# Kernel tuning notes

Measured on AMD Instinct MI355X. Metric: run time of the kernel, lower is better.

## Reference

```python
import jax, jax.numpy as jnp
import numpy as np
import math

B, S, D, H, FF, NB = 32, 512, 512, 8, 2048, 2
DK = D // H  # 64
NEG = -1e30  # stands in for torch's -1e32 (fp32-safe)


def _make_pe():
    # CosinePositionalEmbedding: deterministic sin/cos part (the 0.1*randn is fully overwritten)
    pos = np.arange(S, dtype=np.float32)[:, None]
    div = np.exp(np.arange(0, D, 2, dtype=np.float32) * -(math.log(10000.0) / D))
    pe = np.zeros((S, D), np.float32)
    pe[:, 0::2] = np.sin(pos * div)
    pe[:, 1::2] = np.cos(pos * div)
    return jnp.asarray(pe)[None]  # [1, S, D]


def setup_inputs() -> dict:
    key = jax.random.key(0)
    ks = jax.random.split(key, 10)
    def w(k, shape):
        return jax.random.normal(k, shape, jnp.float32) * 0.02
    return {
        "q_embed_data": jax.random.normal(ks[0], (B, S, D), jnp.float32),
        "qa_embed_data": jax.random.normal(ks[1], (B, S, D), jnp.float32),
        "forget_rate": jax.random.uniform(ks[2], (B, 1, S, 1), jnp.float32),
        "pe": _make_pe(),
        "Wk": w(ks[3], (NB, D, D)), "bk": jnp.zeros((NB, D), jnp.float32),
        "Wv": w(ks[4], (NB, D, D)), "bv": jnp.zeros((NB, D), jnp.float32),
        "Wo": w(ks[5], (NB, D, D)), "bo": jnp.zeros((NB, D), jnp.float32),
        "g1": jnp.ones((NB, D), jnp.float32), "be1": jnp.zeros((NB, D), jnp.float32),
        "W1": w(ks[6], (NB, D, FF)), "bf1": jnp.zeros((NB, FF), jnp.float32),
        "W2": w(ks[7], (NB, FF, D)), "bf2": jnp.zeros((NB, D), jnp.float32),
        "g2": jnp.ones((NB, D), jnp.float32), "be2": jnp.zeros((NB, D), jnp.float32),
    }


def _ln(x, g, b):
    m = jnp.mean(x, axis=-1, keepdims=True)
    v = jnp.var(x, axis=-1, keepdims=True)
    return (x - m) * jax.lax.rsqrt(v + 1e-5) * g + b


def reference(q_embed_data, qa_embed_data, forget_rate, pe, Wk, bk, Wv, bv, Wo, bo,
              g1, be1, W1, bf1, W2, bf2, g2, be2):
    x = q_embed_data + pe[:, :S]   # query stream
    y = qa_embed_data + pe[:, :S]  # value stream (constant across blocks)
    # mask==0 path: src_mask True where triu(k=0)==0, i.e. strictly-past positions j < i
    allowed = jnp.tril(jnp.ones((S, S), bool), k=-1)
    scale = 1.0 / math.sqrt(DK)
    for i in range(NB):
        # kq_same=True: q and k both use k_linear; query=key=x so q == k
        q = (x @ Wk[i] + bk[i]).reshape(B, S, H, DK).transpose(0, 2, 1, 3)  # [B,H,S,dk]
        k = q
        v = (y @ Wv[i] + bv[i]).reshape(B, S, H, DK).transpose(0, 2, 1, 3)
        scores = jnp.einsum('bhqd,bhkd->bhqk', q, k) * scale      # [B,H,S,S]
        scores = scores * forget_rate                              # broadcast [B,1,S,1]
        scores = jnp.where(allowed, scores, NEG)                   # masked_fill(mask==0, -1e32)
        attn = jax.nn.softmax(scores, axis=-1)
        attn = attn.at[:, :, 0, :].set(0.0)                        # zero_pad first query row
        out = jnp.einsum('bhqk,bhkd->bhqd', attn, v)
        out = out.transpose(0, 2, 1, 3).reshape(B, S, D) @ Wo[i] + bo[i]
        x = _ln(x + out, g1[i], be1[i])
        ffn = jax.nn.relu(x @ W1[i] + bf1[i]) @ W2[i] + bf2[i]
        x = _ln(x + ffn, g2[i], be2[i])
    return x
```

## Files before the change

kernel.cpp:

```cpp
#include <hip/hip_runtime.h>

#define B_ 32
#define S_ 512
#define D_ 512
#define H_ 8
#define DK_ 64
#define FF_ 2048

typedef float f32x4 __attribute__((ext_vector_type(4)));
typedef __bf16 bf16x8 __attribute__((ext_vector_type(8)));
typedef __bf16 bf16x4 __attribute__((ext_vector_type(4)));

__device__ __forceinline__ void gld_lds16(const void* gptr, void* lptr) {
    auto g = (__attribute__((address_space(1))) void*)(unsigned long long)gptr;
    auto l = (__attribute__((address_space(3))) void*)(unsigned)(unsigned long long)lptr;
    __builtin_amdgcn_global_load_lds(g, l, 16, 0, 0);
}

__global__ __launch_bounds__(256) void prep_kernel(
    const float* __restrict__ q, const float* __restrict__ qa,
    const float* __restrict__ pe, __bf16* __restrict__ xbf,
    __bf16* __restrict__ ybf)
{
    const int n4 = B_ * S_ * D_ / 4;
    for (int i = blockIdx.x * blockDim.x + threadIdx.x; i < n4;
         i += gridDim.x * blockDim.x) {
        float4 pv = ((const float4*)pe)[i & (S_ * D_ / 4 - 1)];
        float4 qv = ((const float4*)q)[i];
        float4 av = ((const float4*)qa)[i];
        bf16x4 xb = {(__bf16)(qv.x + pv.x), (__bf16)(qv.y + pv.y),
                     (__bf16)(qv.z + pv.z), (__bf16)(qv.w + pv.w)};
        ((bf16x4*)xbf)[i] = xb;
        bf16x4 yb = {(__bf16)(av.x + pv.x), (__bf16)(av.y + pv.y),
                     (__bf16)(av.z + pv.z), (__bf16)(av.w + pv.w)};
        ((bf16x4*)ybf)[i] = yb;
    }
}

__device__ __forceinline__ void ttile(
    const float* __restrict__ in, __bf16* __restrict__ out,
    int R, int C, int bx, int by, int t)
{
    __shared__ float tile[32][33];
    const int tc = bx * 32, tr = by * 32;
    const int lx = t & 31, ly = t >> 5;
    #pragma unroll
    for (int yy = ly; yy < 32; yy += 8)
        tile[yy][lx] = in[(long)(tr + yy) * C + tc + lx];
    __syncthreads();
    #pragma unroll
    for (int yy = ly; yy < 32; yy += 8)
        out[(long)(tc + yy) * R + tr + lx] = (__bf16)tile[lx][yy];
}

__global__ __launch_bounds__(256) void transpose6(
    const float* __restrict__ Wk, const float* __restrict__ Wv,
    const float* __restrict__ Wo, __bf16* __restrict__ ok,
    __bf16* __restrict__ ov, __bf16* __restrict__ oo)
{
    const int z = blockIdx.z, sel = z >> 1, i = z & 1;
    const float* src = sel == 0 ? Wk : (sel == 1 ? Wv : Wo);
    __bf16* dst = sel == 0 ? ok : (sel == 1 ? ov : oo);
    ttile(src + (long)i * 262144, dst + (long)i * 262144, 512, 512,
          blockIdx.x, blockIdx.y, threadIdx.x);
}

__global__ __launch_bounds__(256) void transposeW1(
    const float* __restrict__ W1, __bf16* __restrict__ o1)
{
    const int i = blockIdx.z;
    ttile(W1 + (long)i * 1048576, o1 + (long)i * 1048576, 512, 2048,
          blockIdx.x, blockIdx.y, threadIdx.x);
}

__global__ __launch_bounds__(256) void transposeW2(
    const float* __restrict__ W2, __bf16* __restrict__ o2)
{
    const int i = blockIdx.z;
    ttile(W2 + (long)i * 1048576, o2 + (long)i * 1048576, 2048, 512,
          blockIdx.x, blockIdx.y, threadIdx.x);
}

__global__ __launch_bounds__(256) void vtrans_kernel(
    const __bf16* __restrict__ V, __bf16* __restrict__ Vt)
{
    __shared__ __bf16 tile[64][72];
    const int sb = blockIdx.x, h = blockIdx.y, b = blockIdx.z;
    const int t = threadIdx.x;
    #pragma unroll
    for (int it = 0; it < 16; ++it) {
        int idx = it * 256 + t;
        int rr = idx >> 6, cc = idx & 63;
        tile[cc][rr] = V[((long)(b * S_ + sb * 64 + rr)) * D_ + h * DK_ + cc];
    }
    __syncthreads();
    #pragma unroll
    for (int it = 0; it < 16; ++it) {
        int idx = it * 256 + t;
        int dd = idx >> 6, so = idx & 63;
        Vt[((long)(b * H_ + h) * DK_ + dd) * S_ + sb * 64 + so] = tile[dd][so];
    }
}

template <int RELU, int MODE>
__global__ __launch_bounds__(256) void gemm_kernel(
    const __bf16* __restrict__ A, const __bf16* __restrict__ Bt,
    const float* __restrict__ bias, const __bf16* __restrict__ res,
    __bf16* __restrict__ out, int M, int N, int K)
{
    __shared__ __bf16 As[2][128 * 64];
    __shared__ __bf16 Bs[2][128 * 64];
    const int t = threadIdx.x;
    const int lane = t & 63;
    const int wv = t >> 6, wr = wv >> 1, wc = wv & 1;
    const int lr = lane & 15, lk = lane >> 4;

    const int nwg = gridDim.x * gridDim.y;
    const int lin = blockIdx.y * gridDim.x + blockIdx.x;
    const int swz = (lin & 7) * (nwg >> 3) + (lin >> 3);
    const int m0 = (swz / gridDim.x) * 128, n0 = (swz % gridDim.x) * 128;

    const int srow = t >> 3;
    const int sslot = (t & 7) ^ (srow & 7);
    const __bf16* gA = A + (long)(m0 + srow) * K + sslot * 8;
    const __bf16* gB = Bt + (long)(n0 + srow) * K + sslot * 8;
    const long rstep = (long)32 * K;

    auto STAGE = [&](int bsel, int k0) {
        char* ldsA = (char*)As[bsel] + t * 16;
        char* ldsB = (char*)Bs[bsel] + t * 16;
        #pragma unroll
        for (int u = 0; u < 4; ++u) {
            gld_lds16(gA + u * rstep + k0, ldsA + u * 4096);
            gld_lds16(gB + u * rstep + k0, ldsB + u * 4096);
        }
    };

    f32x4 acc[4][4] = {};
    auto COMPUTE = [&](int bsel) {
        #pragma unroll
        for (int kk = 0; kk < 2; ++kk) {
            bf16x8 af[4], bfr[4];
            #pragma unroll
            for (int i = 0; i < 4; ++i) {
                const int rr = wr * 64 + i * 16 + lr;
                af[i] = *(const bf16x8*)((const char*)As[bsel] +
                        (rr << 7) + (((kk * 4 + lk) ^ (rr & 7)) << 4));
            }
            #pragma unroll
            for (int j = 0; j < 4; ++j) {
                const int rr = wc * 64 + j * 16 + lr;
                bfr[j] = *(const bf16x8*)((const char*)Bs[bsel] +
                         (rr << 7) + (((kk * 4 + lk) ^ (rr & 7)) << 4));
            }
            #pragma unroll
            for (int i = 0; i < 4; ++i)
                #pragma unroll
                for (int j = 0; j < 4; ++j)
                    acc[i][j] = __builtin_amdgcn_mfma_f32_16x16x32_bf16(
                        bfr[j], af[i], acc[i][j], 0, 0, 0);
        }
    };

    const int NT = K >> 6;
    STAGE(0, 0);
    STAGE(1, 64);
    for (int kt = 0; kt < NT - 1; ++kt) {
        asm volatile("s_waitcnt vmcnt(8)" ::: "memory");
        __builtin_amdgcn_s_barrier();
        COMPUTE(kt & 1);
        __builtin_amdgcn_s_barrier();
        if (kt + 2 < NT) STAGE(kt & 1, (kt + 2) << 6);
    }
    asm volatile("s_waitcnt vmcnt(0)" ::: "memory");
    __builtin_amdgcn_s_barrier();
    COMPUTE((NT - 1) & 1);

    #pragma unroll
    for (int i = 0; i < 4; ++i) {
        const int m = m0 + wr * 64 + i * 16 + lr;
        #pragma unroll
        for (int j = 0; j < 4; ++j) {
            const int nb = n0 + wc * 64 + j * 16 + lk * 4;
            const float4 bv = *(const float4*)(bias + nb);
            float v0 = acc[i][j][0] + bv.x;
            float v1 = acc[i][j][1] + bv.y;
            float v2 = acc[i][j][2] + bv.z;
            float v3 = acc[i][j][3] + bv.w;
            if (MODE == 1) {
                const bf16x4 rv = *(const bf16x4*)(res + (long)m * N + nb);
                v0 += (float)rv[0]; v1 += (float)rv[1];
                v2 += (float)rv[2]; v3 += (float)rv[3];
            }
            if (RELU) {
                v0 = v0 > 0.f ? v0 : 0.f; v1 = v1 > 0.f ? v1 : 0.f;
                v2 = v2 > 0.f ? v2 : 0.f; v3 = v3 > 0.f ? v3 : 0.f;
            }
            bf16x4 ov = {(__bf16)v0, (__bf16)v1, (__bf16)v2, (__bf16)v3};
            *(bf16x4*)(out + (long)m * N + nb) = ov;
        }
    }
}

__global__ __launch_bounds__(256) void attn_kernel(
    const __bf16* __restrict__ Q, const __bf16* __restrict__ Vt,
    const float* __restrict__ fr, __bf16* __restrict__ Out)
{
    __shared__ __bf16 Ks[64 * 64];
    __shared__ __bf16 Vs[64 * 64];
    __shared__ __bf16 Plds[4][16 * 64];
    const int t = threadIdx.x;
    const int lane = t & 63, wv = t >> 6;
    const int lr = lane & 15, lk = lane >> 4;
    const int qb = blockIdx.x, h = blockIdx.y, b = blockIdx.z;
    const int qT = qb * 64 + wv * 16;

    const __bf16* qp = Q + (long)(b * S_ + qT + lr) * D_ + h * DK_ + lk * 8;
    const bf16x8 qf0 = *(const bf16x8*)qp;
    const bf16x8 qf1 = *(const bf16x8*)(qp + 32);

    float frv[4], ls[4];
    #pragma unroll
    for (int r = 0; r < 4; ++r) {
        frv[r] = fr[b * S_ + qT + lk * 4 + r] * 0.125f;
        ls[r] = 0.f;
    }
    f32x4 o[4] = {};

    const int srow = t >> 3;
    const int sslot = (t & 7) ^ (srow & 7);
    const __bf16* kstage = Q + (long)(b * S_ + srow) * D_ + h * DK_ + sslot * 8;
    const __bf16* vstage = Vt + ((long)(b * H_ + h) * DK_ + srow) * S_ + sslot * 8;
    char* kd = (char*)Ks + t * 16;
    char* vd = (char*)Vs + t * 16;
    __bf16* pl = &Plds[wv][0];
    const int sw = (lr & 7);

    for (int ks = 0; ks <= qb * 64; ks += 64) {
        gld_lds16(kstage + (long)ks * D_, kd);
        gld_lds16(kstage + (long)(ks + 32) * D_, kd + 4096);
        gld_lds16(vstage + ks, vd);
        gld_lds16(vstage + ks + 32 * S_, vd + 4096);
        __syncthreads();

        f32x4 s[4] = {};
        #pragma unroll
        for (int j = 0; j < 4; ++j) {
            const char* kb = (const char*)Ks + ((j * 16 + lr) << 7);
            const bf16x8 kf0 = *(const bf16x8*)(kb + ((lk ^ sw) << 4));
            const bf16x8 kf1 = *(const bf16x8*)(kb + (((lk + 4) ^ sw) << 4));
            s[j] = __builtin_amdgcn_mfma_f32_16x16x32_bf16(qf0, kf0, s[j], 0, 0, 0);
            s[j] = __builtin_amdgcn_mfma_f32_16x16x32_bf16(qf1, kf1, s[j], 0, 0, 0);
        }
        #pragma unroll
        for (int j = 0; j < 4; ++j) {
            const int col = ks + j * 16 + lr;
            const int c8 = j * 2 + (lr >> 3), cb = lr & 7;
            #pragma unroll
            for (int r = 0; r < 4; ++r) {
                const int row = lk * 4 + r;
                const int sidx = row * 64 + ((c8 ^ (row & 7)) << 3) + cb;
                const float e = __expf(s[j][r] * frv[r]);
                const float p = (col < qT + row) ? e : 0.f;
                ls[r] += p;
                pl[sidx] = (__bf16)p;
            }
        }
        bf16x8 pf[2];
        #pragma unroll
        for (int kk = 0; kk < 2; ++kk) {
            const int ridx = lr * 64 + (((kk * 4 + lk) ^ sw) << 3);
            pf[kk] = *(const bf16x8*)&pl[ridx];
        }
        #pragma unroll
        for (int dt = 0; dt < 4; ++dt) {
            const char* vb = (const char*)Vs + ((dt * 16 + lr) << 7);
            #pragma unroll
            for (int kk = 0; kk < 2; ++kk) {
                const bf16x8 vf = *(const bf16x8*)(vb + (((kk * 4 + lk) ^ sw) << 4));
                o[dt] = __builtin_amdgcn_mfma_f32_16x16x32_bf16(pf[kk], vf, o[dt], 0, 0, 0);
            }
        }
        __syncthreads();
    }

    #pragma unroll
    for (int r = 0; r < 4; ++r) {
        #pragma unroll
        for (int d = 1; d < 16; d <<= 1)
            ls[r] += __shfl_xor(ls[r], d);
        const float inv = ls[r] > 0.f ? 1.f / ls[r] : 0.f;
        #pragma unroll
        for (int dt = 0; dt < 4; ++dt)
            Out[(long)(b * S_ + qT + lk * 4 + r) * D_ + h * DK_ + dt * 16 + lr] =
                (__bf16)(o[dt][r] * inv);
    }
}

__global__ __launch_bounds__(256) void ln_kernel(
    const __bf16* __restrict__ pre, const float* __restrict__ g,
    const float* __restrict__ be, float* __restrict__ xout,
    __bf16* __restrict__ xbf, int wf32)
{
    const int lane = threadIdx.x & 63, wv = threadIdx.x >> 6;
    const long row = (long)blockIdx.x * 4 + wv;
    const bf16x8 v = *(const bf16x8*)(pre + row * D_ + lane * 8);
    float f[8];
    #pragma unroll
    for (int k = 0; k < 8; ++k) f[k] = (float)v[k];
    float s = 0.f, ss = 0.f;
    #pragma unroll
    for (int k = 0; k < 8; ++k) { s += f[k]; ss += f[k] * f[k]; }
    #pragma unroll
    for (int d = 1; d < 64; d <<= 1) {
        s  += __shfl_xor(s, d);
        ss += __shfl_xor(ss, d);
    }
    const float mean = s * (1.f / 512.f);
    const float rstd = rsqrtf(ss * (1.f / 512.f) - mean * mean + 1e-5f);
    const float4 ga = ((const float4*)(g + lane * 8))[0];
    const float4 gc = ((const float4*)(g + lane * 8))[1];
    const float4 ba = ((const float4*)(be + lane * 8))[0];
    const float4 bc = ((const float4*)(be + lane * 8))[1];
    float o[8];
    o[0] = (f[0] - mean) * rstd * ga.x + ba.x;
    o[1] = (f[1] - mean) * rstd * ga.y + ba.y;
    o[2] = (f[2] - mean) * rstd * ga.z + ba.z;
    o[3] = (f[3] - mean) * rstd * ga.w + ba.w;
    o[4] = (f[4] - mean) * rstd * gc.x + bc.x;
    o[5] = (f[5] - mean) * rstd * gc.y + bc.y;
    o[6] = (f[6] - mean) * rstd * gc.z + bc.z;
    o[7] = (f[7] - mean) * rstd * gc.w + bc.w;
    bf16x8 xb = {(__bf16)o[0], (__bf16)o[1], (__bf16)o[2], (__bf16)o[3],
                 (__bf16)o[4], (__bf16)o[5], (__bf16)o[6], (__bf16)o[7]};
    *(bf16x8*)(xbf + row * D_ + lane * 8) = xb;
    if (wf32) {
        float* xo = xout + row * D_ + lane * 8;
        ((float4*)xo)[0] = make_float4(o[0], o[1], o[2], o[3]);
        ((float4*)xo)[1] = make_float4(o[4], o[5], o[6], o[7]);
    }
}

extern "C" void kernel_launch(void* const* d_in, const int* in_sizes, int n_in,
                              void* d_out, int out_size, void* d_ws, size_t ws_size,
                              hipStream_t stream) {
    const float* q_embed = (const float*)d_in[0];
    const float* qa_embed = (const float*)d_in[1];
    const float* fr  = (const float*)d_in[2];
    const float* pe  = (const float*)d_in[3];
    const float* Wk  = (const float*)d_in[4];
    const float* bk  = (const float*)d_in[5];
    const float* Wv  = (const float*)d_in[6];
    const float* bv  = (const float*)d_in[7];
    const float* Wo  = (const float*)d_in[8];
    const float* bo  = (const float*)d_in[9];
    const float* g1  = (const float*)d_in[10];
    const float* be1 = (const float*)d_in[11];
    const float* W1  = (const float*)d_in[12];
    const float* bf1 = (const float*)d_in[13];
    const float* W2  = (const float*)d_in[14];
    const float* bf2 = (const float*)d_in[15];
    const float* g2  = (const float*)d_in[16];
    const float* be2 = (const float*)d_in[17];

    char* ws = (char*)d_ws;
    __bf16* xbf   = (__bf16*)(ws + 0);
    __bf16* ybf   = (__bf16*)(ws + 16777216);
    __bf16* pool  = (__bf16*)(ws + 33554432);
    __bf16* preln = (__bf16*)(ws + 100663296);
    __bf16* wts   = (__bf16*)(ws + 117440512);

    __bf16* kbuf  = pool;
    __bf16* vbuf  = pool + 8388608;
    __bf16* vtbuf = pool + 2 * 8388608;
    __bf16* abuf  = pool + 3 * 8388608;
    __bf16* f1buf = pool;

    __bf16* wkt = wts;
    __bf16* wvt = wts + 524288;
    __bf16* wot = wts + 1048576;
    __bf16* w1t = wts + 1572864;
    __bf16* w2t = wts + 3670016;

    transpose6 <<<dim3(16, 16, 6), 256, 0, stream>>>(Wk, Wv, Wo, wkt, wvt, wot);
    transposeW1<<<dim3(64, 16, 2), 256, 0, stream>>>(W1, w1t);
    transposeW2<<<dim3(16, 64, 2), 256, 0, stream>>>(W2, w2t);
    prep_kernel<<<2048, 256, 0, stream>>>(q_embed, qa_embed, pe, xbf, ybf);

    for (int i = 0; i < 2; ++i) {
        gemm_kernel<0, 0><<<dim3(4, 128), 256, 0, stream>>>(
            xbf, wkt + i * 262144, bk + i * 512, nullptr, kbuf, 16384, 512, 512);
        gemm_kernel<0, 0><<<dim3(4, 128), 256, 0, stream>>>(
            ybf, wvt + i * 262144, bv + i * 512, nullptr, vbuf, 16384, 512, 512);
        vtrans_kernel<<<dim3(8, 8, 32), 256, 0, stream>>>(vbuf, vtbuf);
        attn_kernel<<<dim3(8, 8, 32), 256, 0, stream>>>(kbuf, vtbuf, fr, abuf);
        gemm_kernel<0, 1><<<dim3(4, 128), 256, 0, stream>>>(
            abuf, wot + i * 262144, bo + i * 512, xbf, preln, 16384, 512, 512);
        ln_kernel<<<4096, 256, 0, stream>>>(preln, g1 + i * 512, be1 + i * 512,
                                            (float*)d_out, xbf, 0);
        gemm_kernel<1, 0><<<dim3(16, 128), 256, 0, stream>>>(
            xbf, w1t + i * 1048576, bf1 + i * 2048, nullptr, f1buf, 16384, 2048, 512);
        gemm_kernel<0, 1><<<dim3(4, 128), 256, 0, stream>>>(
            f1buf, w2t + i * 1048576, bf2 + i * 512, xbf, preln, 16384, 512, 2048);
        ln_kernel<<<4096, 256, 0, stream>>>(preln, g2 + i * 512, be2 + i * 512,
                                            (float*)d_out, xbf, i == 1 ? 1 : 0);
    }
}
```

Baseline: 491.2 us.

## Fuse V transpose into V-projection GEMM epilogue via swapped MFMA operands

The V projection GEMM gets a new epilogue mode that writes its output directly in the per-head transposed layout used by attention, removing the separate transpose kernel and its intermediate buffer. To support that, the MFMA operand order is swapped so each lane holds consecutive rows, which changes the epilogue for all GEMMs to scalar bf16 stores and residual loads strided by N. This saves one launch and a full read/write pass of V, but risks less coalesced stores in every other GEMM, including the large FFN ones.

```diff
diff --git a/kernel.cpp b/kernel.cpp
--- a/kernel.cpp
+++ b/kernel.cpp
@@ -81,27 +81,6 @@
           blockIdx.x, blockIdx.y, threadIdx.x);
 }
 
-__global__ __launch_bounds__(256) void vtrans_kernel(
-    const __bf16* __restrict__ V, __bf16* __restrict__ Vt)
-{
-    __shared__ __bf16 tile[64][72];
-    const int sb = blockIdx.x, h = blockIdx.y, b = blockIdx.z;
-    const int t = threadIdx.x;
-    #pragma unroll
-    for (int it = 0; it < 16; ++it) {
-        int idx = it * 256 + t;
-        int rr = idx >> 6, cc = idx & 63;
-        tile[cc][rr] = V[((long)(b * S_ + sb * 64 + rr)) * D_ + h * DK_ + cc];
-    }
-    __syncthreads();
-    #pragma unroll
-    for (int it = 0; it < 16; ++it) {
-        int idx = it * 256 + t;
-        int dd = idx >> 6, so = idx & 63;
-        Vt[((long)(b * H_ + h) * DK_ + dd) * S_ + sb * 64 + so] = tile[dd][so];
-    }
-}
-
 template <int RELU, int MODE>
 __global__ __launch_bounds__(256) void gemm_kernel(
     const __bf16* __restrict__ A, const __bf16* __restrict__ Bt,
@@ -158,7 +137,7 @@
                 #pragma unroll
                 for (int j = 0; j < 4; ++j)
                     acc[i][j] = __builtin_amdgcn_mfma_f32_16x16x32_bf16(
-                        bfr[j], af[i], acc[i][j], 0, 0, 0);
+                        af[i], bfr[j], acc[i][j], 0, 0, 0);
         }
     };
 
@@ -178,26 +157,29 @@
 
     #pragma unroll
     for (int i = 0; i < 4; ++i) {
-        const int m = m0 + wr * 64 + i * 16 + lr;
         #pragma unroll
         for (int j = 0; j < 4; ++j) {
-            const int nb = n0 + wc * 64 + j * 16 + lk * 4;
-            const float4 bv = *(const float4*)(bias + nb);
-            float v0 = acc[i][j][0] + bv.x;
-            float v1 = acc[i][j][1] + bv.y;
-            float v2 = acc[i][j][2] + bv.z;
-            float v3 = acc[i][j][3] + bv.w;
-            if (MODE == 1) {
-                const bf16x4 rv = *(const bf16x4*)(res + (long)m * N + nb);
-                v0 += (float)rv[0]; v1 += (float)rv[1];
-                v2 += (float)rv[2]; v3 += (float)rv[3];
-            }
-            if (RELU) {
-                v0 = v0 > 0.f ? v0 : 0.f; v1 = v1 > 0.f ? v1 : 0.f;
-                v2 = v2 > 0.f ? v2 : 0.f; v3 = v3 > 0.f ? v3 : 0.f;
-            }
-            bf16x4 ov = {(__bf16)v0, (__bf16)v1, (__bf16)v2, (__bf16)v3};
-            *(bf16x4*)(out + (long)m * N + nb) = ov;
+            const int n = n0 + wc * 64 + j * 16 + lr;
+            const float bv = bias[n];
+            if (MODE == 2) {
+                const int mb = m0 + wr * 64 + i * 16 + lk * 4;
+                const int b = mb >> 9, s = mb & 511;
+                bf16x4 ov = {(__bf16)(acc[i][j][0] + bv),
+                             (__bf16)(acc[i][j][1] + bv),
+                             (__bf16)(acc[i][j][2] + bv),
+                             (__bf16)(acc[i][j][3] + bv)};
+                *(bf16x4*)(out + (((long)(b * 8 + (n >> 6)) * 64 + (n & 63)) << 9) + s) = ov;
+            } else {
+                #pragma unroll
+                for (int r = 0; r < 4; ++r) {
+                    const int m = m0 + wr * 64 + i * 16 + lk * 4 + r;
+                    const long off = (long)m * N + n;
+                    float v = acc[i][j][r] + bv;
+                    if (MODE == 1) v += (float)res[off];
+                    if (RELU) v = v > 0.f ? v : 0.f;
+                    out[off] = (__bf16)v;
+                }
+            }
         }
     }
 }
@@ -371,9 +353,8 @@
     __bf16* wts   = (__bf16*)(ws + 117440512);
 
     __bf16* kbuf  = pool;
-    __bf16* vbuf  = pool + 8388608;
-    __bf16* vtbuf = pool + 2 * 8388608;
-    __bf16* abuf  = pool + 3 * 8388608;
+    __bf16* vtbuf = pool + 8388608;
+    __bf16* abuf  = pool + 2 * 8388608;
     __bf16* f1buf = pool;
 
     __bf16* wkt = wts;
@@ -390,9 +371,8 @@
     for (int i = 0; i < 2; ++i) {
         gemm_kernel<0, 0><<<dim3(4, 128), 256, 0, stream>>>(
             xbf, wkt + i * 262144, bk + i * 512, nullptr, kbuf, 16384, 512, 512);
-        gemm_kernel<0, 0><<<dim3(4, 128), 256, 0, stream>>>(
-            ybf, wvt + i * 262144, bv + i * 512, nullptr, vbuf, 16384, 512, 512);
-        vtrans_kernel<<<dim3(8, 8, 32), 256, 0, stream>>>(vbuf, vtbuf);
+        gemm_kernel<0, 2><<<dim3(4, 128), 256, 0, stream>>>(
+            ybf, wvt + i * 262144, bv + i * 512, nullptr, vtbuf, 16384, 512, 512);
         attn_kernel<<<dim3(8, 8, 32), 256, 0, stream>>>(kbuf, vtbuf, fr, abuf);
         gemm_kernel<0, 1><<<dim3(4, 128), 256, 0, stream>>>(
             abuf, wot + i * 262144, bo + i * 512, xbf, preln, 16384, 512, 512);
```

Result: faster. 447.9 us (-8.8%).
